# Optimization experiments

Measured on AMD Instinct MI355X. Metric: run time of the kernel, lower is better.

The kernel has to match this reference:

```python
import jax, jax.numpy as jnp
import numpy as np

CUTOFF = 5.0
RBF_DIM = 20
NUM_GRAPHS = 64
CONV_LAYERS = 3


def envelope(d):
    x = d / CUTOFF
    env = 1.0 - 21.0 * x**5 + 35.0 * x**6 - 15.0 * x**7
    return jnp.where(d < CUTOFF, env, 0.0)


def bessel_rbf(d):
    n = jnp.arange(1, RBF_DIM + 1, dtype=jnp.float32)
    ds = jnp.maximum(d, 1e-6)[:, None]
    return jnp.sqrt(2.0 / CUTOFF) * jnp.sin(n * jnp.pi * ds / CUTOFF) / ds


def spherical_harmonics(bond_vector):
    # normalize=True, normalization='norm'; irreps 64x1e+32x2e -> dim 64*3+32*5=352
    d = jnp.sqrt(jnp.sum(bond_vector**2, axis=-1, keepdims=True) + 1e-12)
    u = bond_vector / d
    x, y, z = u[:, 0], u[:, 1], u[:, 2]
    s3 = jnp.sqrt(jnp.float32(3.0))
    l1 = jnp.stack([y, z, x], axis=-1)                                   # [E,3], unit norm
    l2 = jnp.stack([s3 * x * y, s3 * y * z, 0.5 * (3.0 * z * z - 1.0),
                    s3 * x * z, 0.5 * s3 * (x * x - y * y)], axis=-1)    # [E,5], unit norm
    return jnp.concatenate([jnp.tile(l1, (1, 64)), jnp.tile(l2, (1, 32))], axis=-1)


def setup_inputs():
    key = jax.random.key(0)
    ks = jax.random.split(key, 16)
    N, E, LE, H = 8000, 128000, 512000, 128
    atom_pos = jax.random.uniform(ks[0], (N, 3), dtype=jnp.float32) * 6.0
    edge_attr = jax.random.normal(ks[1], (E, 169), dtype=jnp.float32)
    edge_attr_grad = jax.random.normal(ks[2], (E, 3, 169), dtype=jnp.float32) * 0.1
    edge_index = jax.random.randint(ks[3], (2, E), 0, N)
    neo_edge_index = jax.random.randint(ks[4], (2, LE), 0, E)
    atom_batch = jnp.sort(jax.random.randint(ks[5], (N,), 0, NUM_GRAPHS))
    g = lambda k, shp: jax.random.normal(k, shp, dtype=jnp.float32) / np.sqrt(shp[-2] if len(shp) > 1 else shp[0])
    W_mat = g(ks[6], (169, H)); b_mat = jnp.zeros((H,), jnp.float32)
    W_emb = g(ks[7], (H, H)); b_emb = jnp.zeros((H,), jnp.float32)
    Wv = g(ks[8], (352, H))
    Wr = jax.random.normal(ks[9], (CONV_LAYERS, RBF_DIM, H), dtype=jnp.float32) / np.sqrt(RBF_DIM)
    Wx = jax.random.normal(ks[10], (CONV_LAYERS, H, H), dtype=jnp.float32) / np.sqrt(H)
    w_out = g(ks[11], (H,))
    return {"atom_pos": atom_pos, "edge_attr": edge_attr, "edge_attr_grad": edge_attr_grad,
            "W_mat": W_mat, "b_mat": b_mat, "W_emb": W_emb, "b_emb": b_emb, "Wv": Wv,
            "Wr": Wr, "Wx": Wx, "w_out": w_out, "edge_index": edge_index,
            "neo_edge_index": neo_edge_index, "atom_batch": atom_batch}


def reference(atom_pos, edge_attr, edge_attr_grad, W_mat, b_mat, W_emb, b_emb, Wv, Wr, Wx,
              w_out, edge_index, neo_edge_index, atom_batch):
    N = atom_pos.shape[0]
    E = edge_attr.shape[0]
    src, dst = edge_index[0], edge_index[1]
    le_src, le_dst = neo_edge_index[0], neo_edge_index[1]

    def energy(pos, eattr):
        bond_vector = pos[src] - pos[dst]                                  # [E,3]
        d = jnp.sqrt(jnp.sum(bond_vector**2, axis=-1) + 1e-12)             # [E]
        env = envelope(d)[:, None]                                         # [E,1]
        neo_x = jax.nn.silu((eattr * env) @ W_mat + b_mat) @ W_emb + b_emb  # [E,128]
        rsh = spherical_harmonics(bond_vector)                             # [E,352]
        rbf = bessel_rbf(d)                                                # [E,20]
        # SE3TransformerV2 surrogate: rbf-gated message passing on the edge line graph
        x = neo_x + jax.nn.silu(rsh @ Wv)
        for l in range(CONV_LAYERS):
            gate = jax.nn.silu(rbf @ Wr[l])                                # [E,128]
            m = x[le_src] * gate[le_src]                                   # [LE,128] gather
            agg = jax.ops.segment_sum(m, le_dst, num_segments=E)           # [E,128] scatter
            x = x + jax.nn.silu(agg @ Wx[l])
        e_edge = (x @ w_out) * env[:, 0]                                   # [E]
        node_e = jax.ops.segment_sum(e_edge, src, num_segments=N)          # [N]
        return jax.ops.segment_sum(node_e, atom_batch, num_segments=NUM_GRAPHS)

    results = energy(atom_pos, edge_attr)                                  # [G]
    a_p_g, e_a_g = jax.grad(lambda p, e: jnp.sum(energy(p, e)), argnums=(0, 1))(atom_pos, edge_attr)
    edge_grads = jnp.einsum('ekf,ef->ek', edge_attr_grad, e_a_g)           # [E,3]
    S = jnp.zeros((N, 3), edge_grads.dtype)
    S = S.at[src].add(edge_grads).at[dst].add(-edge_grads)
    force = -(a_p_g + S)                                                   # [N,3]
    return results, force
```

## Files before the change

### kernel.cpp

```cpp
#include <hip/hip_runtime.h>
#include <cstdint>


#define CUTOFF 5.0f
#define PI_F 3.14159265358979323846f

__device__ __forceinline__ float siluf(float v){ float s=1.f/(1.f+__expf(-v)); return v*s; }
__device__ __forceinline__ float silud(float v){ float s=1.f/(1.f+__expf(-v)); return s*(1.f+v*(1.f-s)); }

template<int CTRL>
__device__ __forceinline__ float dpp_radd(float x){
  int y = __builtin_amdgcn_update_dpp(0, __float_as_int(x), CTRL, 0xf, 0xf, false);
  return x + __int_as_float(y);
}
__device__ __forceinline__ float wave_sum63(float x){
  x = dpp_radd<0x111>(x);
  x = dpp_radd<0x112>(x);
  x = dpp_radd<0x114>(x);
  x = dpp_radd<0x118>(x);
  x = dpp_radd<0x142>(x);
  x = dpp_radd<0x143>(x);
  return x;
}

constexpr int PRE_NONE=0, PRE_SCALE_ROW=1, PRE_SILU=2, PRE_MUL_SILUD=3;
constexpr int POST_PLAIN=0, POST_BIAS=1, POST_GATE=2, POST_X0=3, POST_CONV=4, POST_MUL_SILUD=5;

template<int PRE, int POST, bool BT>
__global__ __launch_bounds__(256) void xg_gemm(
    const float* __restrict__ A, int ldA, int K,
    const float* __restrict__ B, int ldB, int N,
    float* __restrict__ C, int ldC,
    const float* __restrict__ rowscale,
    const float* __restrict__ auxA,
    const float* __restrict__ auxC,
    const float* __restrict__ bias,
    const float* __restrict__ l8g,
    const float* __restrict__ Wvsg,
    float* __restrict__ C2,
    int E)
{
  __shared__ float Alds[64][36];
  __shared__ float Blds[32][132];
  __shared__ float l8s[8][64];
  __shared__ float WvsS[8][128];

  const int tid = threadIdx.x;
  const int e0 = blockIdx.x*64;
  const int n0 = blockIdx.y*128;

  if constexpr (POST==POST_X0) {
    for (int i=tid;i<1024;i+=256) WvsS[i>>7][i&127] = Wvsg[i];
    for (int i=tid;i<512;i+=256) {
      int r=i>>3, c=i&7; int e=e0+r;
      l8s[c][r] = (e<E)? l8g[(size_t)e*8+c] : 0.f;
    }
  }

  const int ty = tid>>5, tx = tid&31;
  float acc[8][4];
  #pragma unroll
  for (int i=0;i<8;i++){acc[i][0]=0.f;acc[i][1]=0.f;acc[i][2]=0.f;acc[i][3]=0.f;}

  for (int k0=0;k0<K;k0+=32) {
    __syncthreads();
    {
      const int kk = tid&31, rb = tid>>5;
      #pragma unroll
      for (int p=0;p<8;p++) {
        int r = rb + p*8;
        int e = e0+r, k = k0+kk;
        float v = 0.f;
        if (e<E && k<K) {
          v = A[(size_t)e*ldA + k];
          if constexpr (PRE==PRE_SCALE_ROW) v *= rowscale[e];
          if constexpr (PRE==PRE_SILU)      v = siluf(v);
          if constexpr (PRE==PRE_MUL_SILUD) v *= silud(auxA[(size_t)e*128+k]);
        }
        Alds[r][kk] = v;
      }
    }
    if constexpr (!BT) {
      const int n = tid&127, kb = tid>>7;
      #pragma unroll
      for (int p=0;p<16;p++) {
        int kk = kb + p*2;
        int k = k0+kk, nn = n0+n;
        Blds[kk][n] = (k<K && nn<N) ? B[(size_t)k*ldB+nn] : 0.f;
      }
    } else {
      const int kk = tid&31, nb = tid>>5;
      #pragma unroll
      for (int p=0;p<16;p++) {
        int n = nb + p*8;
        int k = k0+kk, nn = n0+n;
        Blds[kk][n] = (k<K && nn<N) ? B[(size_t)nn*ldB+k] : 0.f;
      }
    }
    __syncthreads();
    #pragma unroll
    for (int kk4=0;kk4<8;kk4++) {
      float4 b0 = *(const float4*)&Blds[kk4*4+0][tx*4];
      float4 b1 = *(const float4*)&Blds[kk4*4+1][tx*4];
      float4 b2 = *(const float4*)&Blds[kk4*4+2][tx*4];
      float4 b3 = *(const float4*)&Blds[kk4*4+3][tx*4];
      #pragma unroll
      for (int i=0;i<8;i++) {
        float4 a = *(const float4*)&Alds[ty*8+i][kk4*4];
        acc[i][0] = fmaf(a.x,b0.x,acc[i][0]);
        acc[i][1] = fmaf(a.x,b0.y,acc[i][1]);
        acc[i][2] = fmaf(a.x,b0.z,acc[i][2]);
        acc[i][3] = fmaf(a.x,b0.w,acc[i][3]);
        acc[i][0] = fmaf(a.y,b1.x,acc[i][0]);
        acc[i][1] = fmaf(a.y,b1.y,acc[i][1]);
        acc[i][2] = fmaf(a.y,b1.z,acc[i][2]);
        acc[i][3] = fmaf(a.y,b1.w,acc[i][3]);
        acc[i][0] = fmaf(a.z,b2.x,acc[i][0]);
        acc[i][1] = fmaf(a.z,b2.y,acc[i][1]);
        acc[i][2] = fmaf(a.z,b2.z,acc[i][2]);
        acc[i][3] = fmaf(a.z,b2.w,acc[i][3]);
        acc[i][0] = fmaf(a.w,b3.x,acc[i][0]);
        acc[i][1] = fmaf(a.w,b3.y,acc[i][1]);
        acc[i][2] = fmaf(a.w,b3.z,acc[i][2]);
        acc[i][3] = fmaf(a.w,b3.w,acc[i][3]);
      }
    }
  }

  const int cbase = n0 + tx*4;
  #pragma unroll
  for (int i=0;i<8;i++) {
    int e = e0 + ty*8 + i;
    if (e>=E) break;
    size_t ci = (size_t)e*ldC + cbase;
    float4 v = make_float4(acc[i][0],acc[i][1],acc[i][2],acc[i][3]);
    if constexpr (POST==POST_BIAS) {
      v.x+=bias[cbase]; v.y+=bias[cbase+1]; v.z+=bias[cbase+2]; v.w+=bias[cbase+3];
      *(float4*)&C[ci]=v;
    } else if constexpr (POST==POST_GATE) {
      float4 xl4 = *(const float4*)&auxC[(size_t)e*128 + cbase];
      v.x=siluf(v.x)*xl4.x; v.y=siluf(v.y)*xl4.y;
      v.z=siluf(v.z)*xl4.z; v.w=siluf(v.w)*xl4.w;
      *(float4*)&C[ci]=v;
    } else if constexpr (POST==POST_X0) {
      float vp0=0.f,vp1=0.f,vp2=0.f,vp3=0.f;
      int r = ty*8+i;
      #pragma unroll
      for (int c=0;c<8;c++){
        float lc = l8s[c][r];
        vp0=fmaf(lc,WvsS[c][cbase+0],vp0); vp1=fmaf(lc,WvsS[c][cbase+1],vp1);
        vp2=fmaf(lc,WvsS[c][cbase+2],vp2); vp3=fmaf(lc,WvsS[c][cbase+3],vp3);
      }
      v.x += bias[cbase+0] + siluf(vp0);
      v.y += bias[cbase+1] + siluf(vp1);
      v.z += bias[cbase+2] + siluf(vp2);
      v.w += bias[cbase+3] + siluf(vp3);
      *(float4*)&C[ci]=v;
    } else if constexpr (POST==POST_CONV) {
      *(float4*)&C[ci]=v;
      float4 xl = *(const float4*)&auxC[(size_t)e*128 + cbase];
      float4 o = make_float4(xl.x+siluf(v.x), xl.y+siluf(v.y),
                             xl.z+siluf(v.z), xl.w+siluf(v.w));
      *(float4*)&C2[ci]=o;
    } else if constexpr (POST==POST_MUL_SILUD) {
      float4 a4 = *(const float4*)&auxC[(size_t)e*128 + cbase];
      v.x*=silud(a4.x); v.y*=silud(a4.y); v.z*=silud(a4.z); v.w*=silud(a4.w);
      *(float4*)&C[ci]=v;
    } else {
      if (cbase+3 < N) { *(float4*)&C[ci]=v; }
      else {
        float vv[4]={v.x,v.y,v.z,v.w};
        #pragma unroll
        for (int j=0;j<4;j++) if (cbase+j<N) C[ci+j]=vv[j];
      }
    }
  }
}

__global__ __launch_bounds__(256) void xg_geom(const float* __restrict__ pos,
  const int* __restrict__ eidx, int E,
  float* __restrict__ bv, float* __restrict__ d_a, float* __restrict__ env_a,
  float* __restrict__ l8, float* __restrict__ rbf)
{
  int e = blockIdx.x*256+threadIdx.x;
  if (e>=E) return;
  int s = eidx[e], t = eidx[E+e];
  float bx = pos[s*3+0]-pos[t*3+0];
  float by = pos[s*3+1]-pos[t*3+1];
  float bz = pos[s*3+2]-pos[t*3+2];
  float d = sqrtf(bx*bx+by*by+bz*bz + 1e-12f);
  bv[(size_t)e*3+0]=bx; bv[(size_t)e*3+1]=by; bv[(size_t)e*3+2]=bz;
  d_a[e]=d;
  float xx = d/CUTOFF;
  float x2=xx*xx, x4=x2*x2, x5=x4*xx, x6=x5*xx, x7=x6*xx;
  env_a[e] = (d<CUTOFF)? (1.f-21.f*x5+35.f*x6-15.f*x7) : 0.f;
  float inv = 1.f/d;
  float ux=bx*inv, uy=by*inv, uz=bz*inv;
  const float s3 = 1.7320508075688772f;
  size_t b8=(size_t)e*8;
  l8[b8+0]=uy; l8[b8+1]=uz; l8[b8+2]=ux;
  l8[b8+3]=s3*ux*uy; l8[b8+4]=s3*uy*uz;
  l8[b8+5]=0.5f*(3.f*uz*uz-1.f);
  l8[b8+6]=s3*ux*uz; l8[b8+7]=0.5f*s3*(ux*ux-uy*uy);
  float ds = fmaxf(d, 1e-6f);
  const float cc = 0.632455532033676f;
  #pragma unroll
  for (int k=0;k<20;k++){
    float th = ((k+1)*PI_F)*ds/CUTOFF;
    rbf[(size_t)e*20+k] = cc*sinf(th)/ds;
  }
}

__global__ void xg_wvs(const float* __restrict__ Wv, float* __restrict__ Wvs){
  int h=threadIdx.x;
  #pragma unroll
  for (int c=0;c<3;c++){
    float s=0.f;
    for (int t=0;t<64;t++) s+=Wv[(size_t)(t*3+c)*128+h];
    Wvs[c*128+h]=s;
  }
  #pragma unroll
  for (int c=0;c<5;c++){
    float s=0.f;
    for (int t=0;t<32;t++) s+=Wv[(size_t)(192+t*5+c)*128+h];
    Wvs[(3+c)*128+h]=s;
  }
}

__global__ __launch_bounds__(256) void xg_hist(const int* __restrict__ nei, int LE,
                                               int* deg_dst, int* deg_src){
  int i=blockIdx.x*256+threadIdx.x;
  if (i>=LE) return;
  atomicAdd(&deg_src[nei[i]],1);
  atomicAdd(&deg_dst[nei[LE+i]],1);
}

__global__ __launch_bounds__(1024) void xg_scan2(const int* __restrict__ degA, int* __restrict__ rpA,
                                                 const int* __restrict__ degB, int* __restrict__ rpB, int n){
  const int* deg = (blockIdx.x==0)? degA : degB;
  int* rp = (blockIdx.x==0)? rpA : rpB;
  __shared__ int wsum[16];
  int tid=threadIdx.x, lane=tid&63, wid=tid>>6;
  int carry=0;
  for (int base=0;base<n;base+=1024){
    int i=base+tid;
    int v=(i<n)?deg[i]:0;
    int x=v;
    #pragma unroll
    for (int off=1;off<64;off<<=1){int y=__shfl_up(x,off); if(lane>=off)x+=y;}
    if (lane==63) wsum[wid]=x;
    __syncthreads();
    if (wid==0 && lane<16){
      int s=wsum[lane];
      #pragma unroll
      for (int off=1;off<16;off<<=1){int y=__shfl_up(s,off); if(lane>=off)s+=y;}
      wsum[lane]=s;
    }
    __syncthreads();
    int woff=(wid==0)?0:wsum[wid-1];
    if (i<n) rp[i]=carry+woff+x-v;
    carry+=wsum[15];
    __syncthreads();
  }
  if (tid==0) rp[n]=carry;
}

__global__ __launch_bounds__(256) void xg_fill(const int* __restrict__ nei, int LE,
    const int* __restrict__ rp_dst, int* cur_dst, int* col_dst,
    const int* __restrict__ rp_src, int* cur_src, int* col_src){
  int i=blockIdx.x*256+threadIdx.x;
  if (i>=LE) return;
  int s=nei[i], d=nei[LE+i];
  int pd = rp_dst[d] + atomicAdd(&cur_dst[d],1);
  col_dst[pd] = s;
  int ps = rp_src[s] + atomicAdd(&cur_src[s],1);
  col_src[ps] = d;
}

__global__ __launch_bounds__(256) void xg_gather1(const float* __restrict__ g,
  const int* __restrict__ rp, const int* __restrict__ col,
  float* __restrict__ out, int E)
{
  const float2* g2 = (const float2*)g;
  float2* out2 = (float2*)out;
  int w=(blockIdx.x*256+threadIdx.x)>>6, lane=threadIdx.x&63;
  int r0 = w*8;
  if (r0>=E) return;
  int s[8], e[8];
  #pragma unroll
  for (int j=0;j<8;j++){
    int r=r0+j;
    s[j]=(r<E)?rp[r]:0; e[j]=(r<E)?rp[r+1]:0;
  }
  float2 acc[8];
  #pragma unroll
  for (int j=0;j<8;j++) acc[j]=make_float2(0.f,0.f);

  int c[8]; float m[8];
  int live=0;
  #pragma unroll
  for (int j=0;j<8;j++){
    bool a = s[j]<e[j]; live |= (int)a;
    c[j]=a?col[s[j]]:0; m[j]=a?1.f:0.f;
  }
  while (live){
    float2 v[8];
    #pragma unroll
    for (int j=0;j<8;j++) v[j]=g2[(size_t)c[j]*64+lane];
    int cn[8]; float mn[8];
    live=0;
    #pragma unroll
    for (int j=0;j<8;j++){
      s[j]++;
      bool a = s[j]<e[j]; live |= (int)a;
      cn[j]=a?col[s[j]]:0; mn[j]=a?1.f:0.f;
    }
    #pragma unroll
    for (int j=0;j<8;j++){
      acc[j].x=fmaf(v[j].x,m[j],acc[j].x); acc[j].y=fmaf(v[j].y,m[j],acc[j].y);
      c[j]=cn[j]; m[j]=mn[j];
    }
  }
  #pragma unroll
  for (int j=0;j<8;j++){
    int r=r0+j;
    if (r<E) out2[(size_t)r*64+lane]=acc[j];
  }
}

__global__ __launch_bounds__(256) void xg_convstream(const float* __restrict__ G,
  const int* , const int* ,
  const float* __restrict__ xl, float* __restrict__ g_x,
  const float* __restrict__ rbf, float* __restrict__ g_rbf,
  const float* __restrict__ Wr_l, int E)
{
  __shared__ float wr[2560];
  for (int i=threadIdx.x;i<2560;i+=256) wr[i]=Wr_l[i];
  __syncthreads();
  const float2* G2 = (const float2*)G;
  const float2* xl2 = (const float2*)xl;
  float2* gx2 = (float2*)g_x;
  const float2* wr2 = (const float2*)wr;
  int w=(blockIdx.x*256+threadIdx.x)>>6, lane=threadIdx.x&63;
  int r0 = w*4;
  if (r0>=E) return;
  #pragma unroll
  for (int j=0;j<4;j++){
    int row=r0+j;
    if (row>=E) break;
    size_t b=(size_t)row*64+lane;
    float2 a = G2[b];
    float2 x2v = xl2[b];
    float rk[20];
    #pragma unroll
    for (int k=0;k<20;k++) rk[k]=rbf[(size_t)row*20+k];
    float gp0=0.f,gp1=0.f;
    #pragma unroll
    for (int k=0;k<20;k++){
      float2 w2=wr2[k*64+lane];
      gp0=fmaf(rk[k],w2.x,gp0); gp1=fmaf(rk[k],w2.y,gp1);
    }
    float ss0=1.f/(1.f+__expf(-gp0)), ss1=1.f/(1.f+__expf(-gp1));
    float gate0=gp0*ss0, gate1=gp1*ss1;
    float sd0=ss0*(1.f+gp0*(1.f-ss0)), sd1=ss1*(1.f+gp1*(1.f-ss1));
    float gg0 = x2v.x*a.x*sd0, gg1 = x2v.y*a.y*sd1;
    float2 gx = gx2[b];
    gx.x += gate0*a.x; gx.y += gate1*a.y;
    gx2[b] = gx;
    #pragma unroll
    for (int k=0;k<20;k++){
      float2 w2=wr2[k*64+lane];
      float v = wave_sum63(fmaf(gg0, w2.x, gg1*w2.y));
      if (lane==63) g_rbf[(size_t)row*20+k] += v;
    }
  }
}

__global__ __launch_bounds__(256) void xg_out(const float* __restrict__ x3,
  const float* __restrict__ env_a, const float* __restrict__ w_out,
  const int* __restrict__ eidx, const int* __restrict__ abatch,
  float* __restrict__ g_env, float* __restrict__ results, int E)
{
  __shared__ float bins[64];
  __shared__ float wsh[128];
  int tid=threadIdx.x;
  if (tid<64) bins[tid]=0.f;
  if (tid<128) wsh[tid]=w_out[tid];
  __syncthreads();
  int lane=tid&63;
  int gw = blockIdx.x*4 + (tid>>6);
  int stride = gridDim.x*4;
  for (int e=gw; e<E; e+=stride){
    size_t b=(size_t)e*128;
    float v = wave_sum63(x3[b+lane]*wsh[lane] + x3[b+lane+64]*wsh[lane+64]);
    if (lane==63){
      g_env[e]=v;
      float ee=v*env_a[e];
      if (ee!=0.f) atomicAdd(&bins[abatch[eidx[e]]], ee);
    }
  }
  __syncthreads();
  if (tid<64){ float bb=bins[tid]; if (bb!=0.f) atomicAdd(&results[tid], bb); }
}

__global__ __launch_bounds__(256) void xg_gxinit(const float* __restrict__ env_a,
  const float* __restrict__ w_out, float* __restrict__ g_x, int E){
  size_t i = (size_t)blockIdx.x*256+threadIdx.x;
  if (i >= (size_t)E*128) return;
  int e = (int)(i>>7), h = (int)(i&127);
  g_x[i] = env_a[e]*w_out[h];
}

__global__ __launch_bounds__(256) void xg_vpath(const float* __restrict__ g_x,
  const float* __restrict__ l8, const float* __restrict__ Wvs,
  float* __restrict__ g_l8, int E)
{
  __shared__ float W[1024];
  for (int i=threadIdx.x;i<1024;i+=256) W[i]=Wvs[i];
  __syncthreads();
  int gw=(blockIdx.x*256+threadIdx.x)>>6, lane=threadIdx.x&63;
  if (gw>=E) return;
  float l[8];
  #pragma unroll
  for (int c=0;c<8;c++) l[c]=l8[(size_t)gw*8+c];
  float vp0=0.f, vp1=0.f;
  #pragma unroll
  for (int c=0;c<8;c++){ vp0=fmaf(l[c],W[c*128+lane],vp0); vp1=fmaf(l[c],W[c*128+lane+64],vp1); }
  size_t b=(size_t)gw*128;
  float gv0 = g_x[b+lane]*silud(vp0);
  float gv1 = g_x[b+lane+64]*silud(vp1);
  #pragma unroll
  for (int c=0;c<8;c++){
    float v = wave_sum63(fmaf(gv0, W[c*128+lane], gv1*W[c*128+lane+64]));
    if (lane==63) g_l8[(size_t)gw*8+c] = v;
  }
}

__global__ __launch_bounds__(256) void xg_eattrbwd(const float* __restrict__ vecb,
  const float* __restrict__ eattr, const float* __restrict__ eagr,
  const float* __restrict__ env_a, float* __restrict__ g_env,
  float* __restrict__ eg, int E)
{
  int gw=(blockIdx.x*256+threadIdx.x)>>6, lane=threadIdx.x&63;
  if (gw>=E) return;
  const float* vr = vecb + (size_t)gw*172;
  const float* ar = eattr + (size_t)gw*169;
  const float* gr = eagr + (size_t)gw*507;
  float se=0.f,e0=0.f,e1=0.f,e2=0.f;
  for (int f=lane; f<169; f+=64){
    float v=vr[f];
    se=fmaf(v,ar[f],se);
    e0=fmaf(v,gr[f],e0);
    e1=fmaf(v,gr[169+f],e1);
    e2=fmaf(v,gr[338+f],e2);
  }
  se=wave_sum63(se); e0=wave_sum63(e0); e1=wave_sum63(e1); e2=wave_sum63(e2);
  if (lane==63){
    g_env[gw] += se;
    float en = env_a[gw];
    eg[(size_t)gw*3+0]=e0*en; eg[(size_t)gw*3+1]=e1*en; eg[(size_t)gw*3+2]=e2*en;
  }
}

__global__ __launch_bounds__(256) void xg_force(const float* __restrict__ bv,
  const float* __restrict__ d_a, const float* __restrict__ g_env,
  const float* __restrict__ g_rbf, const float* __restrict__ g_l8,
  const float* __restrict__ eg, const int* __restrict__ eidx,
  float* __restrict__ force, int E)
{
  int e = blockIdx.x*256+threadIdx.x;
  if (e>=E) return;
  float d = d_a[e];
  float inv = 1.f/d;
  float xx = d/CUTOFF;
  float x2=xx*xx, x4=x2*x2, x5=x4*xx, x6=x5*xx;
  float g_d = g_env[e] * ((d<CUTOFF)? ((-105.f*x4+210.f*x5-105.f*x6)/CUTOFF) : 0.f);
  const float cc=0.632455532033676f;
  float tie = (d>1e-6f)?1.f:0.5f;
  float acc=0.f;
  #pragma unroll
  for (int k=0;k<20;k++){
    float a=(k+1)*PI_F;
    float th=a*d/CUTOFF;
    float sn=sinf(th), cs=cosf(th);
    float drb = cc*((a/CUTOFF)*cs*d - sn)*inv*inv;
    acc = fmaf(g_rbf[(size_t)e*20+k], drb, acc);
  }
  g_d += acc*tie;
  size_t b3=(size_t)e*3, b8=(size_t)e*8;
  float ux=bv[b3+0]*inv, uy=bv[b3+1]*inv, uz=bv[b3+2]*inv;
  const float s3=1.7320508075688772f;
  float G1y=g_l8[b8+0], G1z=g_l8[b8+1], G1x=g_l8[b8+2];
  float A=g_l8[b8+3], B=g_l8[b8+4], Cq=g_l8[b8+5], D=g_l8[b8+6], F=g_l8[b8+7];
  float gux = G1x + s3*(uy*A + uz*D + ux*F);
  float guy = G1y + s3*(ux*A + uz*B) - s3*uy*F;
  float guz = G1z + s3*uy*B + 3.f*uz*Cq + s3*ux*D;
  float ud = ux*gux+uy*guy+uz*guz;
  float gbx = (gux-ux*ud)*inv + g_d*ux;
  float gby = (guy-uy*ud)*inv + g_d*uy;
  float gbz = (guz-uz*ud)*inv + g_d*uz;
  float fx = gbx + eg[b3+0];
  float fy = gby + eg[b3+1];
  float fz = gbz + eg[b3+2];
  int s=eidx[e], t=eidx[E+e];
  atomicAdd(&force[s*3+0],-fx); atomicAdd(&force[s*3+1],-fy); atomicAdd(&force[s*3+2],-fz);
  atomicAdd(&force[t*3+0], fx); atomicAdd(&force[t*3+1], fy); atomicAdd(&force[t*3+2], fz);
}

extern "C" void kernel_launch(void* const* d_in, const int* in_sizes, int n_in,
                              void* d_out, int out_size, void* d_ws, size_t ws_size,
                              hipStream_t stream)
{
  const float* pos   = (const float*)d_in[0];
  const float* eattr = (const float*)d_in[1];
  const float* eagr  = (const float*)d_in[2];
  const float* W_mat = (const float*)d_in[3];
  const float* b_mat = (const float*)d_in[4];
  const float* W_emb = (const float*)d_in[5];
  const float* b_emb = (const float*)d_in[6];
  const float* Wv    = (const float*)d_in[7];
  const float* Wr    = (const float*)d_in[8];
  const float* Wx    = (const float*)d_in[9];
  const float* w_out = (const float*)d_in[10];
  const int* eidx    = (const int*)d_in[11];
  const int* nei     = (const int*)d_in[12];
  const int* abatch  = (const int*)d_in[13];

  const int E  = in_sizes[1]/169;
  const int LE = in_sizes[12]/2;

  float* p = (float*)d_ws;
  auto alloc=[&](size_t n){ float* q=p; p+=n; return q; };
  float* bv    = alloc((size_t)3*E);
  float* d_a   = alloc(E);
  float* env_a = alloc(E);
  float* l8    = alloc((size_t)8*E);
  float* rbf   = alloc((size_t)20*E);
  float* g_env = alloc(E);
  float* g_l8  = alloc((size_t)8*E);
  float* eg    = alloc((size_t)3*E);
  float* Wvs   = alloc(1024);
  float* h_pre = alloc((size_t)128*E);
  float* x0    = alloc((size_t)128*E);
  float* x1    = alloc((size_t)128*E);
  float* x2    = alloc((size_t)128*E);
  float* apre0 = alloc((size_t)128*E);
  float* apre1 = alloc((size_t)128*E);
  float* apre2 = alloc((size_t)128*E);
  float* bufA  = alloc((size_t)128*E);
  float* bufB  = alloc((size_t)128*E);
  float* g_x   = alloc((size_t)128*E);
  float* g_rbf = alloc((size_t)20*E);
  int* ip = (int*)p;
  int* deg_dst = ip; ip+=E;
  int* deg_src = ip; ip+=E;
  int* cur_dst = ip; ip+=E;
  int* cur_src = ip; ip+=E;
  int* rp_dst  = ip; ip+=E+1;
  int* rp_src  = ip; ip+=E+1;
  int* col_dst = ip; ip+=LE;
  int* col_src = ip; ip+=LE;
  float* vecb  = apre0;

  float* results = (float*)d_out;
  float* force   = results + 64;

  hipMemsetAsync(d_out, 0, (size_t)out_size*sizeof(float), stream);
  hipMemsetAsync(g_rbf, 0, (size_t)24*E*sizeof(float), stream);

  float* xsm[4]   = {x0,x1,x2,bufA};
  float* apres[3] = {apre0,apre1,apre2};

  const int gE  = (E+255)/256;
  const int gLE = (LE+255)/256;
  const int gW  = (E+3)/4;
  const int gW4 = (E+15)/16;
  const int gW8 = (E+31)/32;
  dim3 gg((E+63)/64, 1);

  xg_geom<<<gE,256,0,stream>>>(pos, eidx, E, bv, d_a, env_a, l8, rbf);
  xg_wvs<<<1,128,0,stream>>>(Wv, Wvs);
  xg_hist<<<gLE,256,0,stream>>>(nei, LE, deg_dst, deg_src);
  xg_scan2<<<2,1024,0,stream>>>(deg_dst, rp_dst, deg_src, rp_src, E);
  xg_fill<<<gLE,256,0,stream>>>(nei, LE, rp_dst, cur_dst, col_dst, rp_src, cur_src, col_src);

  xg_gemm<PRE_SCALE_ROW,POST_BIAS,false><<<gg,256,0,stream>>>(
      eattr,169,169, W_mat,128,128, h_pre,128, env_a,nullptr,nullptr, b_mat,
      nullptr,nullptr,nullptr, E);
  xg_gemm<PRE_SILU,POST_X0,false><<<gg,256,0,stream>>>(
      h_pre,128,128, W_emb,128,128, x0,128, nullptr,nullptr,nullptr, b_emb,
      l8,Wvs,nullptr, E);

  for (int l=0;l<3;l++) {
    xg_gemm<PRE_NONE,POST_GATE,false><<<gg,256,0,stream>>>(
        rbf,20,20, Wr+(size_t)l*2560,128,128, bufA,128,
        nullptr,nullptr, xsm[l], nullptr,nullptr,nullptr,nullptr, E);
    xg_gather1<<<gW8,256,0,stream>>>(bufA, rp_dst, col_dst, bufB, E);
    xg_gemm<PRE_NONE,POST_CONV,false><<<gg,256,0,stream>>>(
        bufB,128,128, Wx+(size_t)l*16384,128,128, apres[l],128,
        nullptr,nullptr, xsm[l], nullptr,nullptr,nullptr, xsm[l+1], E);
  }

  xg_out<<<512,256,0,stream>>>(bufA, env_a, w_out, eidx, abatch, g_env, results, E);

  xg_gxinit<<<(int)(((size_t)E*128+255)/256),256,0,stream>>>(env_a, w_out, g_x, E);
  for (int l=2;l>=0;l--) {
    xg_gemm<PRE_MUL_SILUD,POST_PLAIN,true><<<gg,256,0,stream>>>(
        g_x,128,128, Wx+(size_t)l*16384,128,128, bufB,128,
        nullptr, apres[l], nullptr, nullptr,nullptr,nullptr,nullptr, E);
    xg_gather1<<<gW8,256,0,stream>>>(bufB, rp_src, col_src, bufA, E);
    xg_convstream<<<gW4,256,0,stream>>>(bufA, nullptr, nullptr, xsm[l], g_x,
                                        rbf, g_rbf, Wr+(size_t)l*2560, E);
  }
  xg_vpath<<<gW,256,0,stream>>>(g_x, l8, Wvs, g_l8, E);
  xg_gemm<PRE_NONE,POST_MUL_SILUD,true><<<gg,256,0,stream>>>(
      g_x,128,128, W_emb,128,128, bufB,128, nullptr,nullptr, h_pre,
      nullptr,nullptr,nullptr,nullptr, E);
  dim3 g8((E+63)/64, 2);
  xg_gemm<PRE_NONE,POST_PLAIN,true><<<g8,256,0,stream>>>(
      bufB,128,128, W_mat,128,169, vecb,172,
      nullptr,nullptr,nullptr,nullptr,nullptr,nullptr,nullptr, E);
  xg_eattrbwd<<<gW,256,0,stream>>>(vecb, eattr, eagr, env_a, g_env, eg, E);
  xg_force<<<gE,256,0,stream>>>(bv, d_a, g_env, g_rbf, g_l8, eg, eidx, force, E);
}
```

Baseline: 3.374 ms.

## Enlarge GEMM tile to 128 rows with 8x8 per-thread register blocking

The shared fused GEMM kernel now covers 128 edge rows per block instead of 64. Each thread computes an 8x8 output micro-tile instead of 8x4, which raises arithmetic per shared-memory read. The global loads for A and B are reworked into float4 vector loads, with scalar fallbacks for unaligned or ragged K. This halves the grid size and adds accumulator register pressure, and the transposed-B path now writes shared memory column by column, which may cause LDS bank conflicts.

```diff
diff --git a/kernel.cpp b/kernel.cpp
--- a/kernel.cpp
+++ b/kernel.cpp
@@ -40,138 +40,178 @@
     float* __restrict__ C2,
     int E)
 {
-  __shared__ float Alds[64][36];
+  __shared__ float Alds[128][36];
   __shared__ float Blds[32][132];
-  __shared__ float l8s[8][64];
+  __shared__ float l8s[8][128];
   __shared__ float WvsS[8][128];
 
   const int tid = threadIdx.x;
-  const int e0 = blockIdx.x*64;
+  const int e0 = blockIdx.x*128;
   const int n0 = blockIdx.y*128;
 
   if constexpr (POST==POST_X0) {
     for (int i=tid;i<1024;i+=256) WvsS[i>>7][i&127] = Wvsg[i];
-    for (int i=tid;i<512;i+=256) {
+    for (int i=tid;i<1024;i+=256) {
       int r=i>>3, c=i&7; int e=e0+r;
       l8s[c][r] = (e<E)? l8g[(size_t)e*8+c] : 0.f;
     }
   }
 
-  const int ty = tid>>5, tx = tid&31;
-  float acc[8][4];
-  #pragma unroll
-  for (int i=0;i<8;i++){acc[i][0]=0.f;acc[i][1]=0.f;acc[i][2]=0.f;acc[i][3]=0.f;}
+  const int tr = tid>>4, tc = tid&15;
+  float acc[8][8];
+  #pragma unroll
+  for (int i=0;i<8;i++)
+    #pragma unroll
+    for (int j=0;j<8;j++) acc[i][j]=0.f;
+
+  const bool alignedA = ((ldA&3)==0);
 
   for (int k0=0;k0<K;k0+=32) {
     __syncthreads();
+    const bool fullK = (k0+32<=K);
     {
-      const int kk = tid&31, rb = tid>>5;
-      #pragma unroll
-      for (int p=0;p<8;p++) {
-        int r = rb + p*8;
-        int e = e0+r, k = k0+kk;
-        float v = 0.f;
-        if (e<E && k<K) {
-          v = A[(size_t)e*ldA + k];
-          if constexpr (PRE==PRE_SCALE_ROW) v *= rowscale[e];
-          if constexpr (PRE==PRE_SILU)      v = siluf(v);
-          if constexpr (PRE==PRE_MUL_SILUD) v *= silud(auxA[(size_t)e*128+k]);
+      const int ra = tid>>1, ha = tid&1;
+      const int e = e0+ra;
+      float rsc = 1.f;
+      if constexpr (PRE==PRE_SCALE_ROW) rsc = (e<E)? rowscale[e] : 0.f;
+      #pragma unroll
+      for (int q=0;q<4;q++){
+        const int kk = ha*16+q*4, k = k0+kk;
+        float4 v = make_float4(0.f,0.f,0.f,0.f);
+        if (e<E) {
+          if (fullK && alignedA) {
+            v = *(const float4*)&A[(size_t)e*ldA + k];
+          } else {
+            if (k+0<K) v.x = A[(size_t)e*ldA + k+0];
+            if (k+1<K) v.y = A[(size_t)e*ldA + k+1];
+            if (k+2<K) v.z = A[(size_t)e*ldA + k+2];
+            if (k+3<K) v.w = A[(size_t)e*ldA + k+3];
+          }
+          if constexpr (PRE==PRE_SCALE_ROW) { v.x*=rsc; v.y*=rsc; v.z*=rsc; v.w*=rsc; }
+          if constexpr (PRE==PRE_SILU) { v.x=siluf(v.x); v.y=siluf(v.y); v.z=siluf(v.z); v.w=siluf(v.w); }
+          if constexpr (PRE==PRE_MUL_SILUD) {
+            float4 ax = *(const float4*)&auxA[(size_t)e*128 + k];
+            v.x*=silud(ax.x); v.y*=silud(ax.y); v.z*=silud(ax.z); v.w*=silud(ax.w);
+          }
         }
-        Alds[r][kk] = v;
+        *(float4*)&Alds[ra][kk] = v;
       }
     }
     if constexpr (!BT) {
-      const int n = tid&127, kb = tid>>7;
-      #pragma unroll
-      for (int p=0;p<16;p++) {
-        int kk = kb + p*2;
-        int k = k0+kk, nn = n0+n;
-        Blds[kk][n] = (k<K && nn<N) ? B[(size_t)k*ldB+nn] : 0.f;
+      const int kb = tid>>3, ng = (tid&7)*16;
+      const int k = k0+kb;
+      #pragma unroll
+      for (int q=0;q<4;q++){
+        float4 v = make_float4(0.f,0.f,0.f,0.f);
+        if (k<K) v = *(const float4*)&B[(size_t)k*ldB + n0 + ng + q*4];
+        *(float4*)&Blds[kb][ng+q*4] = v;
       }
     } else {
-      const int kk = tid&31, nb = tid>>5;
-      #pragma unroll
-      for (int p=0;p<16;p++) {
-        int n = nb + p*8;
-        int k = k0+kk, nn = n0+n;
-        Blds[kk][n] = (k<K && nn<N) ? B[(size_t)nn*ldB+k] : 0.f;
+      const int nb = tid>>1, hb = tid&1;
+      const int nn = n0+nb;
+      #pragma unroll
+      for (int q=0;q<4;q++){
+        const int kk = hb*16+q*4, k = k0+kk;
+        float4 v = make_float4(0.f,0.f,0.f,0.f);
+        if (nn<N) {
+          if (k+3<K) v = *(const float4*)&B[(size_t)nn*ldB + k];
+          else {
+            if (k+0<K) v.x = B[(size_t)nn*ldB + k+0];
+            if (k+1<K) v.y = B[(size_t)nn*ldB + k+1];
+            if (k+2<K) v.z = B[(size_t)nn*ldB + k+2];
+            if (k+3<K) v.w = B[(size_t)nn*ldB + k+3];
+          }
+        }
+        Blds[kk+0][nb]=v.x; Blds[kk+1][nb]=v.y; Blds[kk+2][nb]=v.z; Blds[kk+3][nb]=v.w;
       }
     }
     __syncthreads();
     #pragma unroll
     for (int kk4=0;kk4<8;kk4++) {
-      float4 b0 = *(const float4*)&Blds[kk4*4+0][tx*4];
-      float4 b1 = *(const float4*)&Blds[kk4*4+1][tx*4];
-      float4 b2 = *(const float4*)&Blds[kk4*4+2][tx*4];
-      float4 b3 = *(const float4*)&Blds[kk4*4+3][tx*4];
+      float bb[4][8];
+      #pragma unroll
+      for (int q=0;q<4;q++){
+        float4 x = *(const float4*)&Blds[kk4*4+q][tc*8];
+        float4 y = *(const float4*)&Blds[kk4*4+q][tc*8+4];
+        bb[q][0]=x.x; bb[q][1]=x.y; bb[q][2]=x.z; bb[q][3]=x.w;
+        bb[q][4]=y.x; bb[q][5]=y.y; bb[q][6]=y.z; bb[q][7]=y.w;
+      }
       #pragma unroll
       for (int i=0;i<8;i++) {
-        float4 a = *(const float4*)&Alds[ty*8+i][kk4*4];
-        acc[i][0] = fmaf(a.x,b0.x,acc[i][0]);
-        acc[i][1] = fmaf(a.x,b0.y,acc[i][1]);
-        acc[i][2] = fmaf(a.x,b0.z,acc[i][2]);
-        acc[i][3] = fmaf(a.x,b0.w,acc[i][3]);
-        acc[i][0] = fmaf(a.y,b1.x,acc[i][0]);
-        acc[i][1] = fmaf(a.y,b1.y,acc[i][1]);
-        acc[i][2] = fmaf(a.y,b1.z,acc[i][2]);
-        acc[i][3] = fmaf(a.y,b1.w,acc[i][3]);
-        acc[i][0] = fmaf(a.z,b2.x,acc[i][0]);
-        acc[i][1] = fmaf(a.z,b2.y,acc[i][1]);
-        acc[i][2] = fmaf(a.z,b2.z,acc[i][2]);
-        acc[i][3] = fmaf(a.z,b2.w,acc[i][3]);
-        acc[i][0] = fmaf(a.w,b3.x,acc[i][0]);
-        acc[i][1] = fmaf(a.w,b3.y,acc[i][1]);
-        acc[i][2] = fmaf(a.w,b3.z,acc[i][2]);
-        acc[i][3] = fmaf(a.w,b3.w,acc[i][3]);
+        float4 a = *(const float4*)&Alds[tr*8+i][kk4*4];
+        float av[4]={a.x,a.y,a.z,a.w};
+        #pragma unroll
+        for (int q=0;q<4;q++)
+          #pragma unroll
+          for (int j=0;j<8;j++)
+            acc[i][j] = fmaf(av[q], bb[q][j], acc[i][j]);
       }
     }
   }
 
-  const int cbase = n0 + tx*4;
+  const int cb = n0 + tc*8;
   #pragma unroll
   for (int i=0;i<8;i++) {
-    int e = e0 + ty*8 + i;
+    int e = e0 + tr*8 + i;
     if (e>=E) break;
-    size_t ci = (size_t)e*ldC + cbase;
-    float4 v = make_float4(acc[i][0],acc[i][1],acc[i][2],acc[i][3]);
+    size_t ci = (size_t)e*ldC + cb;
+    float4 lo = make_float4(acc[i][0],acc[i][1],acc[i][2],acc[i][3]);
+    float4 hi = make_float4(acc[i][4],acc[i][5],acc[i][6],acc[i][7]);
     if constexpr (POST==POST_BIAS) {
-      v.x+=bias[cbase]; v.y+=bias[cbase+1]; v.z+=bias[cbase+2]; v.w+=bias[cbase+3];
-      *(float4*)&C[ci]=v;
+      float4 b0 = *(const float4*)&bias[cb];
+      float4 b1 = *(const float4*)&bias[cb+4];
+      lo.x+=b0.x; lo.y+=b0.y; lo.z+=b0.z; lo.w+=b0.w;
+      hi.x+=b1.x; hi.y+=b1.y; hi.z+=b1.z; hi.w+=b1.w;
+      *(float4*)&C[ci]=lo; *(float4*)&C[ci+4]=hi;
     } else if constexpr (POST==POST_GATE) {
-      float4 xl4 = *(const float4*)&auxC[(size_t)e*128 + cbase];
-      v.x=siluf(v.x)*xl4.x; v.y=siluf(v.y)*xl4.y;
-      v.z=siluf(v.z)*xl4.z; v.w=siluf(v.w)*xl4.w;
-      *(float4*)&C[ci]=v;
+      float4 x0v = *(const float4*)&auxC[(size_t)e*128 + cb];
+      float4 x1v = *(const float4*)&auxC[(size_t)e*128 + cb+4];
+      lo.x=siluf(lo.x)*x0v.x; lo.y=siluf(lo.y)*x0v.y; lo.z=siluf(lo.z)*x0v.z; lo.w=siluf(lo.w)*x0v.w;
+      hi.x=siluf(hi.x)*x1v.x; hi.y=siluf(hi.y)*x1v.y; hi.z=siluf(hi.z)*x1v.z; hi.w=siluf(hi.w)*x1v.w;
+      *(float4*)&C[ci]=lo; *(float4*)&C[ci+4]=hi;
     } else if constexpr (POST==POST_X0) {
-      float vp0=0.f,vp1=0.f,vp2=0.f,vp3=0.f;
-      int r = ty*8+i;
+      int r = tr*8+i;
+      float vp[8];
+      #pragma unroll
+      for (int j=0;j<8;j++) vp[j]=0.f;
       #pragma unroll
       for (int c=0;c<8;c++){
         float lc = l8s[c][r];
-        vp0=fmaf(lc,WvsS[c][cbase+0],vp0); vp1=fmaf(lc,WvsS[c][cbase+1],vp1);
-        vp2=fmaf(lc,WvsS[c][cbase+2],vp2); vp3=fmaf(lc,WvsS[c][cbase+3],vp3);
+        float4 w0 = *(const float4*)&WvsS[c][cb];
+        float4 w1 = *(const float4*)&WvsS[c][cb+4];
+        vp[0]=fmaf(lc,w0.x,vp[0]); vp[1]=fmaf(lc,w0.y,vp[1]);
+        vp[2]=fmaf(lc,w0.z,vp[2]); vp[3]=fmaf(lc,w0.w,vp[3]);
+        vp[4]=fmaf(lc,w1.x,vp[4]); vp[5]=fmaf(lc,w1.y,vp[5]);
+        vp[6]=fmaf(lc,w1.z,vp[6]); vp[7]=fmaf(lc,w1.w,vp[7]);
       }
-      v.x += bias[cbase+0] + siluf(vp0);
-      v.y += bias[cbase+1] + siluf(vp1);
-      v.z += bias[cbase+2] + siluf(vp2);
-      v.w += bias[cbase+3] + siluf(vp3);
-      *(float4*)&C[ci]=v;
+      float4 b0 = *(const float4*)&bias[cb];
+      float4 b1 = *(const float4*)&bias[cb+4];
+      lo.x += b0.x + siluf(vp[0]); lo.y += b0.y + siluf(vp[1]);
+      lo.z += b0.z + siluf(vp[2]); lo.w += b0.w + siluf(vp[3]);
+      hi.x += b1.x + siluf(vp[4]); hi.y += b1.y + siluf(vp[5]);
+      hi.z += b1.z + siluf(vp[6]); hi.w += b1.w + siluf(vp[7]);
+      *(float4*)&C[ci]=lo; *(float4*)&C[ci+4]=hi;
     } else if constexpr (POST==POST_CONV) {
-      *(float4*)&C[ci]=v;
-      float4 xl = *(const float4*)&auxC[(size_t)e*128 + cbase];
-      float4 o = make_float4(xl.x+siluf(v.x), xl.y+siluf(v.y),
-                             xl.z+siluf(v.z), xl.w+siluf(v.w));
-      *(float4*)&C2[ci]=o;
+      *(float4*)&C[ci]=lo; *(float4*)&C[ci+4]=hi;
+      float4 x0v = *(const float4*)&auxC[(size_t)e*128 + cb];
+      float4 x1v = *(const float4*)&auxC[(size_t)e*128 + cb+4];
+      float4 o0 = make_float4(x0v.x+siluf(lo.x), x0v.y+siluf(lo.y),
+                              x0v.z+siluf(lo.z), x0v.w+siluf(lo.w));
+      float4 o1 = make_float4(x1v.x+siluf(hi.x), x1v.y+siluf(hi.y),
+                              x1v.z+siluf(hi.z), x1v.w+siluf(hi.w));
+      *(float4*)&C2[ci]=o0; *(float4*)&C2[ci+4]=o1;
     } else if constexpr (POST==POST_MUL_SILUD) {
-      float4 a4 = *(const float4*)&auxC[(size_t)e*128 + cbase];
-      v.x*=silud(a4.x); v.y*=silud(a4.y); v.z*=silud(a4.z); v.w*=silud(a4.w);
-      *(float4*)&C[ci]=v;
+      float4 a0 = *(const float4*)&auxC[(size_t)e*128 + cb];
+      float4 a1 = *(const float4*)&auxC[(size_t)e*128 + cb+4];
+      lo.x*=silud(a0.x); lo.y*=silud(a0.y); lo.z*=silud(a0.z); lo.w*=silud(a0.w);
+      hi.x*=silud(a1.x); hi.y*=silud(a1.y); hi.z*=silud(a1.z); hi.w*=silud(a1.w);
+      *(float4*)&C[ci]=lo; *(float4*)&C[ci+4]=hi;
     } else {
-      if (cbase+3 < N) { *(float4*)&C[ci]=v; }
+      if (cb+7 < N) { *(float4*)&C[ci]=lo; *(float4*)&C[ci+4]=hi; }
       else {
-        float vv[4]={v.x,v.y,v.z,v.w};
+        float vv[8]={lo.x,lo.y,lo.z,lo.w,hi.x,hi.y,hi.z,hi.w};
         #pragma unroll
-        for (int j=0;j<4;j++) if (cbase+j<N) C[ci+j]=vv[j];
+        for (int j=0;j<8;j++) if (cb+j<N) C[ci+j]=vv[j];
       }
     }
   }
@@ -576,7 +616,7 @@
   const int gW  = (E+3)/4;
   const int gW4 = (E+15)/16;
   const int gW8 = (E+31)/32;
-  dim3 gg((E+63)/64, 1);
+  dim3 gg((E+127)/128, 1);
 
   xg_geom<<<gE,256,0,stream>>>(pos, eidx, E, bv, d_a, env_a, l8, rbf);
   xg_wvs<<<1,128,0,stream>>>(Wv, Wvs);
@@ -616,7 +656,7 @@
   xg_gemm<PRE_NONE,POST_MUL_SILUD,true><<<gg,256,0,stream>>>(
       g_x,128,128, W_emb,128,128, bufB,128, nullptr,nullptr, h_pre,
       nullptr,nullptr,nullptr,nullptr, E);
-  dim3 g8((E+63)/64, 2);
+  dim3 g8((E+127)/128, 2);
   xg_gemm<PRE_NONE,POST_PLAIN,true><<<g8,256,0,stream>>>(
       bufB,128,128, W_mat,128,169, vecb,172,
       nullptr,nullptr,nullptr,nullptr,nullptr,nullptr,nullptr, E);
```

Result: faster. 2.794 ms (-17.2%).
